# Performance work log

Measured on AMD Instinct MI355X. Metric: run time of the kernel, lower is better.

## Reference

```python
import jax, jax.numpy as jnp
import numpy as np

CHANNELS, STYLE_DIM, N_HEADS, N_TOK = 512, 256, 2, 50
HEAD_DIM = STYLE_DIM // N_HEADS
SCALE = STYLE_DIM ** (-0.5)


def setup_inputs() -> dict:
    key = jax.random.key(0)
    ks = jax.random.split(key, 12)
    B, T = 16, 4096
    s = lambda fan_in: 1.0 / np.sqrt(fan_in)
    return {
        "x": jax.random.normal(ks[0], (B, CHANNELS, T), jnp.float32),
        "style": jax.random.normal(ks[1], (B, N_TOK, STYLE_DIM), jnp.float32),
        "key_emb": jax.random.normal(ks[2], (1, N_TOK, STYLE_DIM), jnp.float32) * 0.3,
        "Wq": jax.random.uniform(ks[3], (STYLE_DIM, CHANNELS), jnp.float32, -s(CHANNELS), s(CHANNELS)),
        "bq": jax.random.uniform(ks[4], (STYLE_DIM,), jnp.float32, -s(CHANNELS), s(CHANNELS)),
        "Wk": jax.random.uniform(ks[5], (STYLE_DIM, STYLE_DIM), jnp.float32, -s(STYLE_DIM), s(STYLE_DIM)),
        "bk": jax.random.uniform(ks[6], (STYLE_DIM,), jnp.float32, -s(STYLE_DIM), s(STYLE_DIM)),
        "Wv": jax.random.uniform(ks[7], (STYLE_DIM, STYLE_DIM), jnp.float32, -s(STYLE_DIM), s(STYLE_DIM)),
        "bv": jax.random.uniform(ks[8], (STYLE_DIM,), jnp.float32, -s(STYLE_DIM), s(STYLE_DIM)),
        "Wo": jax.random.uniform(ks[9], (CHANNELS, STYLE_DIM), jnp.float32, -s(STYLE_DIM), s(STYLE_DIM)),
        "bo": jax.random.uniform(ks[10], (CHANNELS,), jnp.float32, -s(STYLE_DIM), s(STYLE_DIM)),
    }


def reference(x, style, key_emb, Wq, bq, Wk, bk, Wv, bv, Wo, bo):
    B, C, T = x.shape
    N = style.shape[1]
    # Q from x (transposed to [B,T,C]); K from static learned embedding; V from style
    q = jnp.einsum('bct,dc->btd', x, Wq) + bq                 # [B,T,style_dim]
    k = jnp.einsum('bns,ds->bnd', jnp.broadcast_to(key_emb, (B, N_TOK, STYLE_DIM)), Wk) + bk
    v = jnp.einsum('bns,ds->bnd', style, Wv) + bv
    # split heads: [B,H,T,hd] / [B,H,N,hd]
    q = q.reshape(B, T, N_HEADS, HEAD_DIM).transpose(0, 2, 1, 3)
    k = k.reshape(B, N_TOK, N_HEADS, HEAD_DIM).transpose(0, 2, 1, 3)
    v = v.reshape(B, N, N_HEADS, HEAD_DIM).transpose(0, 2, 1, 3)
    # tanh applied to transposed keys before QK^T
    attn = jnp.einsum('bhtd,bhnd->bhtn', q, jnp.tanh(k)) * SCALE
    attn = jax.nn.softmax(attn, axis=-1)
    out = jnp.einsum('bhtn,bhnd->bhtd', attn, v)              # [B,H,T,hd]
    out = out.transpose(0, 2, 1, 3).reshape(B, T, STYLE_DIM)
    out = jnp.einsum('btd,cd->btc', out, Wo) + bo             # [B,T,C]
    return x + out.transpose(0, 2, 1)
```

## Files before the change

kernel.cpp:

```cpp
#include <hip/hip_runtime.h>
#include <stdint.h>

#define CHN 512
#define TDIM 4096
#define SD 256
#define HD 128
#define NTOK 50
#define NP 64
#define NB 16
#define TT 64
#define QPITCH 264
#define XPITCH 132
#define YPITCH 66
#define SCALE_ 0.0625f

typedef float f32x4 __attribute__((ext_vector_type(4)));
typedef unsigned int u32x4 __attribute__((ext_vector_type(4)));
typedef short s16x8 __attribute__((ext_vector_type(8)));

__device__ __forceinline__ uint16_t f2bf(float f) {
  union { float f; uint32_t u; } v; v.f = f;
  uint32_t r = (v.u + 0x7fffu + ((v.u >> 16) & 1u)) >> 16;
  return (uint16_t)r;
}
__device__ __forceinline__ uint32_t packbf(float lo, float hi) {
  return (uint32_t)f2bf(lo) | ((uint32_t)f2bf(hi) << 16);
}
__device__ __forceinline__ void mfma_bf16(f32x4& d, u32x4 a, u32x4 b) {
  union { u32x4 u; s16x8 s; } ua, ub;
  ua.u = a; ub.u = b;
  d = __builtin_amdgcn_mfma_f32_16x16x32_bf16(ua.s, ub.s, d, 0, 0, 0);
}

__global__ void conv_w_kernel(const float* __restrict__ Wq, const float* __restrict__ Wo,
                              uint16_t* __restrict__ wqb, uint16_t* __restrict__ wob) {
  int i = blockIdx.x * 256 + threadIdx.x;
  wqb[i] = f2bf(Wq[i]);
  wob[i] = f2bf(Wo[i]);
}

__global__ void prep_kv_kernel(const float* __restrict__ style, const float* __restrict__ kemb,
                               const float* __restrict__ Wk, const float* __restrict__ bk,
                               const float* __restrict__ Wv, const float* __restrict__ bv,
                               uint16_t* __restrict__ kt, uint16_t* __restrict__ vT) {
  int id = blockIdx.x * 256 + threadIdx.x;
  if (id < 2 * NP * HD) {
    int dh = id & (HD - 1);
    int n  = (id >> 7) & (NP - 1);
    int h  = id >> 13;
    uint16_t r = 0;
    if (n < NTOK) {
      int d = h * HD + dh;
      float acc = bk[d];
      const float* er = kemb + (size_t)n * SD;
      const float* wr = Wk + (size_t)d * SD;
      for (int s = 0; s < SD; s += 4) {
        float4 e = *(const float4*)(er + s);
        float4 w4 = *(const float4*)(wr + s);
        acc += e.x * w4.x + e.y * w4.y + e.z * w4.z + e.w * w4.w;
      }
      r = f2bf(tanhf(acc));
    }
    kt[id] = r;
  } else {
    int vid = id - 2 * NP * HD;
    int n  = vid & (NP - 1);
    int dh = (vid >> 6) & (HD - 1);
    int h  = (vid >> 13) & 1;
    int bb = vid >> 14;
    uint16_t r = 0;
    if (n < NTOK) {
      int d = h * HD + dh;
      float acc = bv[d];
      const float* sr = style + (size_t)(bb * NTOK + n) * SD;
      const float* wr = Wv + (size_t)d * SD;
      for (int s = 0; s < SD; s += 4) {
        float4 e = *(const float4*)(sr + s);
        float4 w4 = *(const float4*)(wr + s);
        acc += e.x * w4.x + e.y * w4.y + e.z * w4.z + e.w * w4.w;
      }
      r = f2bf(acc);
    }
    vT[vid] = r;
  }
}

__global__ __launch_bounds__(256, 2) void qproj_attn_kernel(
    const float* __restrict__ x, const float* __restrict__ bq,
    const uint16_t* __restrict__ wqb,
    const uint16_t* __restrict__ kt, const uint16_t* __restrict__ vT,
    uint16_t* __restrict__ o) {
  __shared__ uint16_t qs[TT * QPITCH];

  const int bb = blockIdx.y;
  const int t0 = blockIdx.x * TT;
  const int tid = threadIdx.x;
  const int lane = tid & 63;
  const int w = tid >> 6;
  const int l15 = lane & 15;
  const int g = lane >> 4;

  const float* xb = x + (size_t)bb * CHN * TDIM + t0;

  f32x4 acc[4][4];
#pragma unroll
  for (int mt = 0; mt < 4; ++mt)
#pragma unroll
    for (int nt = 0; nt < 4; ++nt) acc[mt][nt] = (f32x4){0.f, 0.f, 0.f, 0.f};

  const int tse = (tid & 31) << 1;
  const int cb  = (tid >> 5) << 1;

  float2 va[8], vb[8];
#pragma unroll
  for (int p = 0; p < 8; ++p) {
    int c = cb + 16 * p;
    va[p] = *(const float2*)(xb + (size_t)c * TDIM + tse);
    vb[p] = *(const float2*)(xb + (size_t)(c + 1) * TDIM + tse);
  }

  for (int cc = 0; cc < 4; ++cc) {
    const int c0 = cc * 128;
    __syncthreads();
#pragma unroll
    for (int p = 0; p < 8; ++p) {
      int cl = cb + 16 * p;
      *(uint32_t*)&qs[tse * XPITCH + cl]       = packbf(va[p].x, vb[p].x);
      *(uint32_t*)&qs[(tse + 1) * XPITCH + cl] = packbf(va[p].y, vb[p].y);
    }
    if (cc < 3) {
      const int c0n = c0 + 128;
#pragma unroll
      for (int p = 0; p < 8; ++p) {
        int c = c0n + cb + 16 * p;
        va[p] = *(const float2*)(xb + (size_t)c * TDIM + tse);
        vb[p] = *(const float2*)(xb + (size_t)(c + 1) * TDIM + tse);
      }
    }
    __syncthreads();
#pragma unroll
    for (int ks = 0; ks < 4; ++ks) {
      u32x4 afr[4];
#pragma unroll
      for (int mt = 0; mt < 4; ++mt) {
        int dr = (w * 4 + mt) * 16 + l15;
        afr[mt] = *(const u32x4*)(wqb + (size_t)dr * CHN + c0 + ks * 32 + g * 8);
      }
#pragma unroll
      for (int nt = 0; nt < 4; ++nt) {
        int tr = nt * 16 + l15;
        const uint16_t* pb = &qs[tr * XPITCH + ks * 32 + g * 8];
        uint2 lo = *(const uint2*)pb;
        uint2 hi = *(const uint2*)(pb + 4);
        u32x4 bfr = (u32x4){lo.x, lo.y, hi.x, hi.y};
#pragma unroll
        for (int mt = 0; mt < 4; ++mt) mfma_bf16(acc[mt][nt], afr[mt], bfr);
      }
    }
  }
  __syncthreads();
#pragma unroll
  for (int mt = 0; mt < 4; ++mt) {
    int d0 = (w * 4 + mt) * 16 + g * 4;
    float4 bqv = *(const float4*)(bq + d0);
#pragma unroll
    for (int nt = 0; nt < 4; ++nt) {
      int tr = nt * 16 + l15;
      uint2 wv;
      wv.x = packbf(acc[mt][nt][0] + bqv.x, acc[mt][nt][1] + bqv.y);
      wv.y = packbf(acc[mt][nt][2] + bqv.z, acc[mt][nt][3] + bqv.w);
      *(uint2*)&qs[tr * QPITCH + d0] = wv;
    }
  }
  __syncthreads();

  const int tmy = w * 16 + l15;
  const uint16_t* qrow = &qs[tmy * QPITCH];
  uint16_t* og = o + (size_t)(bb * TDIM + t0 + tmy) * SD;
  const int l1 = l15 + 16 * ((2 * g) & 3);
  const int l2 = l15 + 16 * ((2 * g + 1) & 3);
  const bool hiH = (g >> 1) != 0;

#pragma unroll
  for (int h = 0; h < 2; ++h) {
    u32x4 bq4[4];
#pragma unroll
    for (int ks = 0; ks < 4; ++ks)
      bq4[ks] = *(const u32x4*)(qrow + h * HD + ks * 32 + g * 8);

    f32x4 sac[4];
#pragma unroll
    for (int mtn = 0; mtn < 4; ++mtn) {
      sac[mtn] = (f32x4){0.f, 0.f, 0.f, 0.f};
#pragma unroll
      for (int ks = 0; ks < 4; ++ks) {
        u32x4 afr = *(const u32x4*)(kt + (size_t)(h * NP + mtn * 16 + l15) * HD + ks * 32 + g * 8);
        mfma_bf16(sac[mtn], afr, bq4[ks]);
      }
    }
    float pv[4][4];
    float mx = -3.0e38f;
#pragma unroll
    for (int mtn = 0; mtn < 4; ++mtn)
#pragma unroll
      for (int j = 0; j < 4; ++j) {
        int n = mtn * 16 + g * 4 + j;
        float s = (n < NTOK) ? sac[mtn][j] * SCALE_ : -3.0e38f;
        pv[mtn][j] = s;
        mx = fmaxf(mx, s);
      }
    mx = fmaxf(mx, __shfl_xor(mx, 16, 64));
    mx = fmaxf(mx, __shfl_xor(mx, 32, 64));
    float sum = 0.f;
#pragma unroll
    for (int mtn = 0; mtn < 4; ++mtn)
#pragma unroll
      for (int j = 0; j < 4; ++j) {
        float e = __expf(pv[mtn][j] - mx);
        pv[mtn][j] = e;
        sum += e;
      }
    sum += __shfl_xor(sum, 16, 64);
    sum += __shfl_xor(sum, 32, 64);
    float inv = 1.0f / sum;
    uint32_t pk[4][2];
#pragma unroll
    for (int mtn = 0; mtn < 4; ++mtn) {
      pk[mtn][0] = packbf(pv[mtn][0] * inv, pv[mtn][1] * inv);
      pk[mtn][1] = packbf(pv[mtn][2] * inv, pv[mtn][3] * inv);
    }
    u32x4 bp[2];
#pragma unroll
    for (int ks = 0; ks < 2; ++ks) {
      uint32_t a0 = (uint32_t)__shfl((int)pk[2 * ks][0], l1, 64);
      uint32_t b0 = (uint32_t)__shfl((int)pk[2 * ks + 1][0], l1, 64);
      uint32_t a1 = (uint32_t)__shfl((int)pk[2 * ks][1], l1, 64);
      uint32_t b1 = (uint32_t)__shfl((int)pk[2 * ks + 1][1], l1, 64);
      uint32_t a2 = (uint32_t)__shfl((int)pk[2 * ks][0], l2, 64);
      uint32_t b2 = (uint32_t)__shfl((int)pk[2 * ks + 1][0], l2, 64);
      uint32_t a3 = (uint32_t)__shfl((int)pk[2 * ks][1], l2, 64);
      uint32_t b3 = (uint32_t)__shfl((int)pk[2 * ks + 1][1], l2, 64);
      bp[ks] = (u32x4){hiH ? b0 : a0, hiH ? b1 : a1, hiH ? b2 : a2, hiH ? b3 : a3};
    }
    const uint16_t* vb2 = vT + (size_t)((bb * 2 + h) * HD) * NP;
#pragma unroll
    for (int mtd = 0; mtd < 8; ++mtd) {
      f32x4 oac = (f32x4){0.f, 0.f, 0.f, 0.f};
#pragma unroll
      for (int ks = 0; ks < 2; ++ks) {
        u32x4 afr = *(const u32x4*)(vb2 + (size_t)(mtd * 16 + l15) * NP + ks * 32 + g * 8);
        mfma_bf16(oac, afr, bp[ks]);
      }
      int d0 = h * HD + mtd * 16 + g * 4;
      uint2 wv;
      wv.x = packbf(oac[0], oac[1]);
      wv.y = packbf(oac[2], oac[3]);
      *(uint2*)(og + d0) = wv;
    }
  }
}

__global__ void oproj_kernel(
    const float* __restrict__ x, const float* __restrict__ bo,
    const uint16_t* __restrict__ wob, const uint16_t* __restrict__ o,
    float* __restrict__ out) {
  __shared__ float ys[128 * YPITCH];
  const int bb = blockIdx.y;
  const int t0 = blockIdx.x * TT;
  const int c0q = blockIdx.z * 128;
  const int tid = threadIdx.x;
  const int lane = tid & 63;
  const int w = tid >> 6;
  const int l15 = lane & 15;
  const int g = lane >> 4;
  const int tmy = w * 16 + l15;

  const uint16_t* orow_in = o + (size_t)(bb * TDIM + t0 + tmy) * SD;
  u32x4 ak[8];
#pragma unroll
  for (int ks = 0; ks < 8; ++ks)
    ak[ks] = *(const u32x4*)(orow_in + ks * 32 + g * 8);

#pragma unroll
  for (int nt = 0; nt < 8; ++nt) {
    int cl = nt * 16 + l15;
    const uint16_t* wrow = wob + (size_t)(c0q + cl) * SD;
    f32x4 yac = (f32x4){0.f, 0.f, 0.f, 0.f};
#pragma unroll
    for (int ks = 0; ks < 8; ++ks) {
      u32x4 bfr = *(const u32x4*)(wrow + ks * 32 + g * 8);
      mfma_bf16(yac, ak[ks], bfr);
    }
    *(f32x4*)&ys[cl * YPITCH + w * 16 + g * 4] = yac;
  }
  __syncthreads();

  const int ct = tid >> 4;
  const int tl = (tid & 15) * 4;
  const float* xr = x + (size_t)bb * CHN * TDIM;
  float* orow = out + (size_t)bb * CHN * TDIM;
#pragma unroll
  for (int it = 0; it < 8; ++it) {
    int cl = ct + it * 16;
    int c = c0q + cl;
    float4 yv = *(float4*)&ys[cl * YPITCH + tl];
    float4 xv = *(const float4*)(xr + (size_t)c * TDIM + t0 + tl);
    float bov = bo[c];
    float4 ov;
    ov.x = xv.x + yv.x + bov;
    ov.y = xv.y + yv.y + bov;
    ov.z = xv.z + yv.z + bov;
    ov.w = xv.w + yv.w + bov;
    *(float4*)(orow + (size_t)c * TDIM + t0 + tl) = ov;
  }
}

extern "C" void kernel_launch(void* const* d_in, const int* in_sizes, int n_in,
                              void* d_out, int out_size, void* d_ws, size_t ws_size,
                              hipStream_t stream) {
  const float* x     = (const float*)d_in[0];
  const float* style = (const float*)d_in[1];
  const float* kemb  = (const float*)d_in[2];
  const float* Wq    = (const float*)d_in[3];
  const float* bq    = (const float*)d_in[4];
  const float* Wk    = (const float*)d_in[5];
  const float* bk    = (const float*)d_in[6];
  const float* Wv    = (const float*)d_in[7];
  const float* bv    = (const float*)d_in[8];
  const float* Wo    = (const float*)d_in[9];
  const float* bo    = (const float*)d_in[10];
  float* out = (float*)d_out;

  uint16_t* wqb = (uint16_t*)d_ws;
  uint16_t* wob = wqb + 131072;
  uint16_t* ktw = wob + 131072;
  uint16_t* vTw = ktw + 16384;
  uint16_t* ob  = vTw + 262144;

  conv_w_kernel<<<512, 256, 0, stream>>>(Wq, Wo, wqb, wob);
  prep_kv_kernel<<<1088, 256, 0, stream>>>(style, kemb, Wk, bk, Wv, bv, ktw, vTw);
  dim3 grid(TDIM / TT, NB);
  qproj_attn_kernel<<<grid, 256, 0, stream>>>(x, bq, wqb, ktw, vTw, ob);
  dim3 gridC(TDIM / TT, NB, 4);
  oproj_kernel<<<gridC, 256, 0, stream>>>(x, bo, wob, ob, out);
}
```

Measured before the change: 265.6 us.

## Split output projection into bf16 y-compute kernel and streaming residual-add kernel

The fused output-projection-plus-residual kernel is split in two. The first kernel computes Wo·o per tile and stores the result as packed bf16 to a workspace buffer. The second is a grid-stride elementwise kernel that adds x, the unpacked y and the bias. The aim is to decouple the MFMA phase from the strided residual read/write. In exchange it adds a full bf16 round trip of y through global memory and an extra launch, and rounds the projection output to bf16.

Measured after the change: 323.3 us. 1.22x slower.

```diff
diff --git a/kernel.cpp b/kernel.cpp
--- a/kernel.cpp
+++ b/kernel.cpp
@@ -11,7 +11,7 @@
 #define TT 64
 #define QPITCH 264
 #define XPITCH 132
-#define YPITCH 66
+#define YUP 34
 #define SCALE_ 0.0625f
 
 typedef float f32x4 __attribute__((ext_vector_type(4)));
@@ -260,11 +260,10 @@
   }
 }
 
-__global__ void oproj_kernel(
-    const float* __restrict__ x, const float* __restrict__ bo,
+__global__ void ycomp_kernel(
     const uint16_t* __restrict__ wob, const uint16_t* __restrict__ o,
-    float* __restrict__ out) {
-  __shared__ float ys[128 * YPITCH];
+    uint32_t* __restrict__ y) {
+  __shared__ uint32_t ys[128 * YUP];
   const int bb = blockIdx.y;
   const int t0 = blockIdx.x * TT;
   const int c0q = blockIdx.z * 128;
@@ -291,27 +290,39 @@
       u32x4 bfr = *(const u32x4*)(wrow + ks * 32 + g * 8);
       mfma_bf16(yac, ak[ks], bfr);
     }
-    *(f32x4*)&ys[cl * YPITCH + w * 16 + g * 4] = yac;
+    uint2 pk2;
+    pk2.x = packbf(yac[0], yac[1]);
+    pk2.y = packbf(yac[2], yac[3]);
+    *(uint2*)&ys[cl * YUP + w * 8 + g * 2] = pk2;
   }
   __syncthreads();
 
-  const int ct = tid >> 4;
-  const int tl = (tid & 15) * 4;
-  const float* xr = x + (size_t)bb * CHN * TDIM;
-  float* orow = out + (size_t)bb * CHN * TDIM;
-#pragma unroll
-  for (int it = 0; it < 8; ++it) {
-    int cl = ct + it * 16;
-    int c = c0q + cl;
-    float4 yv = *(float4*)&ys[cl * YPITCH + tl];
-    float4 xv = *(const float4*)(xr + (size_t)c * TDIM + t0 + tl);
+  const int r = tid >> 1;
+  const int hf = (tid & 1) * 16;
+  const uint32_t* src = &ys[r * YUP + hf];
+  uint32_t* dst = y + ((size_t)(bb * CHN + c0q + r) * TDIM + t0) / 2 + hf;
+#pragma unroll
+  for (int k = 0; k < 4; ++k)
+    *(u32x4*)(dst + k * 4) = *(const u32x4*)(src + k * 4);
+}
+
+__global__ void resid_kernel(
+    const float* __restrict__ x, const uint32_t* __restrict__ y,
+    const float* __restrict__ bo, float* __restrict__ out) {
+  const size_t N4 = (size_t)NB * CHN * TDIM / 4;
+  size_t i = (size_t)blockIdx.x * blockDim.x + threadIdx.x;
+  const size_t stride = (size_t)gridDim.x * blockDim.x;
+  for (; i < N4; i += stride) {
+    float4 xv = *(const float4*)(x + i * 4);
+    uint2 yv = *(const uint2*)(y + i * 2);
+    int c = (int)((i >> 10) & (CHN - 1));
     float bov = bo[c];
     float4 ov;
-    ov.x = xv.x + yv.x + bov;
-    ov.y = xv.y + yv.y + bov;
-    ov.z = xv.z + yv.z + bov;
-    ov.w = xv.w + yv.w + bov;
-    *(float4*)(orow + (size_t)c * TDIM + t0 + tl) = ov;
+    ov.x = xv.x + __uint_as_float(yv.x << 16)          + bov;
+    ov.y = xv.y + __uint_as_float(yv.x & 0xffff0000u)  + bov;
+    ov.z = xv.z + __uint_as_float(yv.y << 16)          + bov;
+    ov.w = xv.w + __uint_as_float(yv.y & 0xffff0000u)  + bov;
+    *(float4*)(out + i * 4) = ov;
   }
 }
 
@@ -336,11 +347,13 @@
   uint16_t* ktw = wob + 131072;
   uint16_t* vTw = ktw + 16384;
   uint16_t* ob  = vTw + 262144;
+  uint32_t* yb  = (uint32_t*)(ob + 16777216);
 
   conv_w_kernel<<<512, 256, 0, stream>>>(Wq, Wo, wqb, wob);
   prep_kv_kernel<<<1088, 256, 0, stream>>>(style, kemb, Wk, bk, Wv, bv, ktw, vTw);
   dim3 grid(TDIM / TT, NB);
   qproj_attn_kernel<<<grid, 256, 0, stream>>>(x, bq, wqb, ktw, vTw, ob);
   dim3 gridC(TDIM / TT, NB, 4);
-  oproj_kernel<<<gridC, 256, 0, stream>>>(x, bo, wob, ob, out);
-}
+  ycomp_kernel<<<gridC, 256, 0, stream>>>(wob, ob, yb);
+  resid_kernel<<<2048, 256, 0, stream>>>(x, yb, bo, out);
+}
```
